# Kernel optimization log

Measured on AMD Instinct MI355X. Metric: run time of the kernel, lower is better.

Reference implementation:

```python
import jax, jax.numpy as jnp
import numpy as np

LEN = 8388608  # 2**23, must be a power of 2


def setup_inputs() -> dict:
    key = jax.random.key(0)
    k1, k2 = jax.random.split(key)
    inp = jax.random.normal(k1, (LEN,), dtype=jnp.float32)
    weight = jax.random.uniform(k2, (LEN // 2, 2), dtype=jnp.float32)  # learned twiddle factors
    return {"input": inp, "weight": weight}


def _complex_mul(a, w):
    # a: [d, cols, 2] complex pairs; w: [cols, 2] broadcast over leading dim
    ar, ai = a[:, :, 0], a[:, :, 1]
    wr, wi = w[:, 0], w[:, 1]
    return jnp.stack([ar * wr - ai * wi, ar * wi + ai * wr], axis=-1)


def reference(input, weight):
    n = input.shape[0]
    # real signal -> complex pairs, shape [n, 1, 2]
    x = jnp.stack([input, jnp.zeros_like(input)], axis=-1)[:, None, :]
    d = n // 2
    while d != 0:  # log2(n) static stages
        w = weight[0::d]          # [cols, 2] where cols == x.shape[1]
        top = x[:d]               # [d, cols, 2]
        bot = x[d:]               # [d, cols, 2]
        p = _complex_mul(bot, w)  # butterfly twiddle multiply
        x = jnp.concatenate([top + p, top - p], axis=1)  # [d, 2*cols, 2]
        d //= 2
    return x  # [1, n, 2]
```

## Files before the change

kernel.cpp:

```cpp
#include <hip/hip_runtime.h>
#include <hip/hip_fp16.h>

typedef float    f4 __attribute__((ext_vector_type(4)));
typedef unsigned u4 __attribute__((ext_vector_type(4)));

__device__ __forceinline__ float2 cadd(float2 a, float2 b) { return make_float2(a.x + b.x, a.y + b.y); }
__device__ __forceinline__ float2 csub(float2 a, float2 b) { return make_float2(a.x - b.x, a.y - b.y); }
__device__ __forceinline__ float2 cmul(float2 w, float2 z) {
    return make_float2(w.x * z.x - w.y * z.y, w.x * z.y + w.y * z.x);
}
__device__ __forceinline__ unsigned pk(float2 z) {
    __half2 h = __floats2half2_rn(z.x, z.y);
    return *reinterpret_cast<unsigned*>(&h);
}
__device__ __forceinline__ float2 upk(unsigned u) {
    __half2 h = *reinterpret_cast<__half2*>(&u);
    return __half22float2(h);
}

__host__ __device__ constexpr unsigned crev(unsigned x, int bits) {
    unsigned r = 0;
    for (int k = 0; k < bits; ++k) r |= ((x >> k) & 1u) << (bits - 1 - k);
    return r;
}


__global__ __launch_bounds__(256) void fft_pass_a(const float* __restrict__ in,
                                                  const float2* __restrict__ wt,
                                                  uint4* __restrict__ outp)
{
    __shared__ float2 L[4096];
    const int tid = threadIdx.x;
    const int l0  = blockIdx.x << 4;
    const int c   = tid & 15;
    const int qb  = tid >> 4;

    float2 pw1[4], pw2a[4], pw2b[4];
#pragma unroll
    for (int k = 0; k < 4; ++k) { pw1[k] = wt[0]; pw2a[k] = wt[0]; pw2b[k] = wt[1 << 21]; }

    {
        const int c4 = tid & 3, gg = tid >> 2;
#pragma unroll
        for (int k = 0; k < 4; ++k) {
            const int g = gg + (k << 6);
            const f4 v = __builtin_nontemporal_load(
                reinterpret_cast<const f4*>(in + ((size_t)g << 15) + l0 + (c4 << 2)));
            const int base = (g << 4) + (c4 << 2);
            L[base + 0] = make_float2(v[0], 0.f);
            L[base + 1] = make_float2(v[1], 0.f);
            L[base + 2] = make_float2(v[2], 0.f);
            L[base + 3] = make_float2(v[3], 0.f);
        }
    }
    __syncthreads();

#pragma unroll
    for (int rho = 0; rho < 4; ++rho) {
        const int s = rho << 1, H = 128 >> s, Q = H >> 1, lo = 6 - s;
        float2 nw1[4], nw2a[4], nw2b[4];
        if (rho < 3) {
            const int s2 = s + 2, lo2 = 6 - s2;
#pragma unroll
            for (int k = 0; k < 4; ++k) {
                const int qi = (qb << 2) + k;
                const int b  = ((qi >> lo2) << (lo2 + 2)) | (qi & ((1 << lo2) - 1));
                const int jl = (int)(__brev((unsigned)(b >> (8 - s2))) >> (32 - s2));
                const int e  = jl << (21 - s2);
                nw1[k] = wt[e << 1]; nw2a[k] = wt[e]; nw2b[k] = wt[e + (1 << 21)];
            }
        }
#pragma unroll
        for (int k = 0; k < 4; ++k) {
            const int qi = (qb << 2) + k;
            const int b  = ((qi >> lo) << (lo + 2)) | (qi & ((1 << lo) - 1));
            const int iA = (b << 4) + c;
            const float2 A  = L[iA];
            const float2 Bv = L[iA + (Q << 4)];
            const float2 Cv = L[iA + (H << 4)];
            const float2 Dv = L[iA + ((H + Q) << 4)];
            const float2 pC = cmul(pw1[k], Cv), pD = cmul(pw1[k], Dv);
            const float2 tA = cadd(A, pC),  tC = csub(A, pC);
            const float2 tB = cadd(Bv, pD), tD = csub(Bv, pD);
            const float2 p2 = cmul(pw2a[k], tB);
            const float2 p3 = cmul(pw2b[k], tD);
            L[iA]                  = cadd(tA, p2);
            L[iA + (Q << 4)]       = csub(tA, p2);
            L[iA + (H << 4)]       = cadd(tC, p3);
            L[iA + ((H + Q) << 4)] = csub(tC, p3);
        }
        __syncthreads();
        if (rho < 3) {
#pragma unroll
            for (int k = 0; k < 4; ++k) { pw1[k] = nw1[k]; pw2a[k] = nw2a[k]; pw2b[k] = nw2b[k]; }
        }
    }

    {
        const int c4 = tid & 3, gg = tid >> 2;
#pragma unroll
        for (int k = 0; k < 4; ++k) {
            const int g  = gg + (k << 6);
            const int li = (g << 4) + (c4 << 2);
            u4 v;
            v[0] = pk(L[li]); v[1] = pk(L[li + 1]); v[2] = pk(L[li + 2]); v[3] = pk(L[li + 3]);
            __builtin_nontemporal_store(v,
                reinterpret_cast<u4*>(&outp[((size_t)g << 13) + (l0 >> 2) + c4]));
        }
    }
}

__global__ __launch_bounds__(256) void fft_pass_b(const unsigned* __restrict__ in,
                                                  const float2* __restrict__ wt,
                                                  unsigned* __restrict__ out)
{
    const int tid = threadIdx.x;
    const int h   = blockIdx.x >> 2;
    const int low = ((blockIdx.x & 3) << 8) | tid;
    const unsigned hrev = __brev((unsigned)h) >> 24;
    const unsigned base = ((unsigned)h << 15) | (unsigned)low;

    float2 X[32];
#pragma unroll
    for (int m = 0; m < 32; ++m)
        X[m] = upk(__builtin_nontemporal_load(&in[base + ((unsigned)m << 10)]));

#pragma unroll
    for (int s = 0; s < 5; ++s) {
        const int half = 1 << (4 - s);
#pragma unroll
        for (int j = 0; j < 16; ++j) {
            const int mh = j >> (4 - s);
            const int lo = (mh << (5 - s)) | (j & (half - 1));
            const int hi = lo | half;
            const unsigned cr = crev((unsigned)mh, s);
            const float2 w = wt[(((cr << 8) | hrev) << (14 - s))];
            const float2 p = cmul(w, X[hi]);
            X[hi] = csub(X[lo], p);
            X[lo] = cadd(X[lo], p);
        }
    }
#pragma unroll
    for (int m = 0; m < 32; ++m)
        __builtin_nontemporal_store(pk(X[m]), &out[base + ((unsigned)m << 10)]);
}

__global__ __launch_bounds__(1024, 8) void fft_pass_c(const uint4* __restrict__ inp4,
                                                      const float2* __restrict__ wt,
                                                      float2* __restrict__ out)
{
    extern __shared__ float2 L[];
    const int tid = threadIdx.x;
    const int bid = blockIdx.x;
    const int h0  = ((bid & 7) << 7) | (bid >> 3);
    const int lam = tid & 7;
    const int bq  = tid >> 3;
    const int R   = (h0 << 3) | lam;

    {
        const int f    = tid & 63;
        const int lm   = (tid >> 6) & 7;
        const int half = tid >> 9;
        const unsigned H = __brev((unsigned)((h0 << 3) | lm)) >> 19;
        const size_t gb = ((size_t)H << 8);
#pragma unroll
        for (int k = 0; k < 2; ++k) {
            const int slot = (half << 7) | (k << 6) | f;
            const u4 v = __builtin_nontemporal_load(
                reinterpret_cast<const u4*>(&inp4[gb + slot]));
            const int base = lm * 1026 + (slot << 2);
            const float2 e0 = upk(v[0]), e1 = upk(v[1]), e2 = upk(v[2]), e3 = upk(v[3]);
            *reinterpret_cast<float4*>(&L[base])     = make_float4(e0.x, e0.y, e1.x, e1.y);
            *reinterpret_cast<float4*>(&L[base + 2]) = make_float4(e2.x, e2.y, e3.x, e3.y);
        }
    }

    float2 w1[2], w2a[2], w2b[2];
#pragma unroll
    for (int k = 0; k < 2; ++k) {
        const int e = R << 8;
        w1[k] = wt[e << 1]; w2a[k] = wt[e]; w2b[k] = wt[e + (1 << 21)];
    }
    float2 f1[2], f2a[2], f2b[2];
    __syncthreads();

#pragma unroll
    for (int rho = 0; rho < 4; ++rho) {
        const int sh = 8 - (rho << 1);
        const int Q  = 1 << sh;
        const int H2 = Q << 1;
        float2 nw1[2], nw2a[2], nw2b[2];
        if (rho < 3) {
            const int rn = rho + 1, shn = 8 - (rn << 1);
#pragma unroll
            for (int k = 0; k < 2; ++k) {
                const int qi = (k << 7) | bq;
                const unsigned ar = (unsigned)(qi >> shn);
                const unsigned xr = __brev(ar) >> (32 - (rn << 1));
                const int e = (int)(((xr << 13) | (unsigned)R) << shn);
                nw1[k] = wt[e << 1]; nw2a[k] = wt[e]; nw2b[k] = wt[e + (1 << 21)];
            }
        } else {
#pragma unroll
            for (int k = 0; k < 2; ++k) {
                const int qi = (k << 7) | bq;
                const unsigned xr = __brev((unsigned)qi) >> 24;
                const int e = (int)((xr << 13) | (unsigned)R);
                f1[k] = wt[e << 1]; f2a[k] = wt[e]; f2b[k] = wt[e + (1 << 21)];
            }
        }
#pragma unroll
        for (int k = 0; k < 2; ++k) {
            const int qi = (k << 7) | bq;
            const int x  = ((qi >> sh) << (sh + 2)) | (qi & (Q - 1));
            const int iA = lam * 1026 + x;
            const float2 A  = L[iA];
            const float2 Bv = L[iA + Q];
            const float2 Cv = L[iA + H2];
            const float2 Dv = L[iA + H2 + Q];
            const float2 pC = cmul(w1[k], Cv), pD = cmul(w1[k], Dv);
            const float2 tA = cadd(A, pC),  tC = csub(A, pC);
            const float2 tB = cadd(Bv, pD), tD = csub(Bv, pD);
            const float2 p2 = cmul(w2a[k], tB);
            const float2 p3 = cmul(w2b[k], tD);
            L[iA]           = cadd(tA, p2);
            L[iA + Q]       = csub(tA, p2);
            L[iA + H2]      = cadd(tC, p3);
            L[iA + H2 + Q]  = csub(tC, p3);
        }
        __syncthreads();
        if (rho < 3) {
#pragma unroll
            for (int k = 0; k < 2; ++k) { w1[k] = nw1[k]; w2a[k] = nw2a[k]; w2b[k] = nw2b[k]; }
        }
    }

    {
#pragma unroll
        for (int k = 0; k < 2; ++k) {
            const int qi = (k << 7) | bq;
            const int x  = qi << 2;
            const int iA = lam * 1026 + x;
            const float4 g0 = *reinterpret_cast<const float4*>(&L[iA]);
            const float4 g1 = *reinterpret_cast<const float4*>(&L[iA + 2]);
            const float2 A  = make_float2(g0.x, g0.y);
            const float2 Bv = make_float2(g0.z, g0.w);
            const float2 Cv = make_float2(g1.x, g1.y);
            const float2 Dv = make_float2(g1.z, g1.w);
            const float2 pC = cmul(f1[k], Cv), pD = cmul(f1[k], Dv);
            const float2 tA = cadd(A, pC),  tC = csub(A, pC);
            const float2 tB = cadd(Bv, pD), tD = csub(Bv, pD);
            const float2 p2 = cmul(f2a[k], tB);
            const float2 p3 = cmul(f2b[k], tD);
            const float2 rA = cadd(tA, p2), rB = csub(tA, p2);
            const float2 rC = cadd(tC, p3), rD = csub(tC, p3);
            *reinterpret_cast<float4*>(&L[iA])     = make_float4(rA.x, rA.y, rB.x, rB.y);
            *reinterpret_cast<float4*>(&L[iA + 2]) = make_float4(rC.x, rC.y, rD.x, rD.y);
        }
    }
    __syncthreads();

    {
        const int l2   = (tid & 3) << 1;
        const int rest = tid >> 2;
#pragma unroll
        for (int k = 0; k < 4; ++k) {
            const int x = (k << 8) | rest;
            const float2 a0 = L[l2 * 1026 + x];
            const float2 a1 = L[(l2 + 1) * 1026 + x];
            const size_t o = ((size_t)(__brev((unsigned)x) >> 22) << 13)
                           | (unsigned)((h0 << 3) | l2);
            f4 sv; sv[0] = a0.x; sv[1] = a0.y; sv[2] = a1.x; sv[3] = a1.y;
            __builtin_nontemporal_store(sv, reinterpret_cast<f4*>(out + o));
        }
    }
}

extern "C" void kernel_launch(void* const* d_in, const int* in_sizes, int n_in,
                              void* d_out, int out_size, void* d_ws, size_t ws_size,
                              hipStream_t stream)
{
    (void)in_sizes; (void)n_in; (void)out_size; (void)ws_size;
    const float*  in = (const float*)d_in[0];
    const float2* wt = (const float2*)d_in[1];
    float2* outc = (float2*)d_out;
    uint4*  buf1 = (uint4*)d_ws;
    unsigned* buf2 = (unsigned*)((char*)d_ws + (32u << 20));

    static bool attr_done = false;
    if (!attr_done) {
        (void)hipFuncSetAttribute(reinterpret_cast<const void*>(fft_pass_c),
                                  hipFuncAttributeMaxDynamicSharedMemorySize, 8 * 1026 * 8);
        attr_done = true;
    }

    fft_pass_a<<<2048, 256, 0, stream>>>(in, wt, buf1);
    fft_pass_b<<<1024, 256, 0, stream>>>((const unsigned*)buf1, wt, buf2);
    fft_pass_c<<<1024, 1024, 8 * 1026 * 8, stream>>>((const uint4*)buf2, wt, outc);
}
```

Before: 201.7 us.

## Rework final FFT pass to one wavefront per row with register and shuffle butterflies

The last FFT pass now gives each 1024-point row to a single 64-lane wavefront. Each lane holds 16 elements in registers, so the first four stages run inside registers and the last six use cross-lane shuffles, instead of radix-4 passes through shared memory with block-wide barriers. Shared memory is kept only for the final transpose and bit-reversed store, and the block size drops to 512 threads. The trade-off is more per-lane twiddle loads, some of them selected per lane, plus higher register pressure and lower thread count per block.

```diff
diff --git a/kernel.cpp b/kernel.cpp
--- a/kernel.cpp
+++ b/kernel.cpp
@@ -22,6 +22,16 @@
     unsigned r = 0;
     for (int k = 0; k < bits; ++k) r |= ((x >> k) & 1u) << (bits - 1 - k);
     return r;
+}
+
+__device__ __forceinline__ float2 sbfly(float2 x, int m, bool hi, float s, float2 wv) {
+    float2 o;
+    o.x = __shfl_xor(x.x, m);
+    o.y = __shfl_xor(x.y, m);
+    const float2 a = hi ? o : x;
+    const float2 b = hi ? x : o;
+    const float2 p = cmul(wv, b);
+    return make_float2(fmaf(s, p.x, a.x), fmaf(s, p.y, a.y));
 }
 
 
@@ -145,127 +155,142 @@
         __builtin_nontemporal_store(pk(X[m]), &out[base + ((unsigned)m << 10)]);
 }
 
-__global__ __launch_bounds__(1024, 8) void fft_pass_c(const uint4* __restrict__ inp4,
-                                                      const float2* __restrict__ wt,
-                                                      float2* __restrict__ out)
+__global__ __launch_bounds__(512, 4) void fft_pass_c(const unsigned* __restrict__ inp,
+                                                     const float2* __restrict__ wt,
+                                                     float2* __restrict__ out)
 {
     extern __shared__ float2 L[];
-    const int tid = threadIdx.x;
-    const int bid = blockIdx.x;
-    const int h0  = ((bid & 7) << 7) | (bid >> 3);
-    const int lam = tid & 7;
-    const int bq  = tid >> 3;
-    const int R   = (h0 << 3) | lam;
-
-    {
-        const int f    = tid & 63;
-        const int lm   = (tid >> 6) & 7;
-        const int half = tid >> 9;
-        const unsigned H = __brev((unsigned)((h0 << 3) | lm)) >> 19;
-        const size_t gb = ((size_t)H << 8);
-#pragma unroll
-        for (int k = 0; k < 2; ++k) {
-            const int slot = (half << 7) | (k << 6) | f;
-            const u4 v = __builtin_nontemporal_load(
-                reinterpret_cast<const u4*>(&inp4[gb + slot]));
-            const int base = lm * 1026 + (slot << 2);
-            const float2 e0 = upk(v[0]), e1 = upk(v[1]), e2 = upk(v[2]), e3 = upk(v[3]);
-            *reinterpret_cast<float4*>(&L[base])     = make_float4(e0.x, e0.y, e1.x, e1.y);
-            *reinterpret_cast<float4*>(&L[base + 2]) = make_float4(e2.x, e2.y, e3.x, e3.y);
-        }
-    }
-
-    float2 w1[2], w2a[2], w2b[2];
-#pragma unroll
-    for (int k = 0; k < 2; ++k) {
-        const int e = R << 8;
-        w1[k] = wt[e << 1]; w2a[k] = wt[e]; w2b[k] = wt[e + (1 << 21)];
-    }
-    float2 f1[2], f2a[2], f2b[2];
-    __syncthreads();
-
-#pragma unroll
-    for (int rho = 0; rho < 4; ++rho) {
-        const int sh = 8 - (rho << 1);
-        const int Q  = 1 << sh;
-        const int H2 = Q << 1;
-        float2 nw1[2], nw2a[2], nw2b[2];
-        if (rho < 3) {
-            const int rn = rho + 1, shn = 8 - (rn << 1);
-#pragma unroll
-            for (int k = 0; k < 2; ++k) {
-                const int qi = (k << 7) | bq;
-                const unsigned ar = (unsigned)(qi >> shn);
-                const unsigned xr = __brev(ar) >> (32 - (rn << 1));
-                const int e = (int)(((xr << 13) | (unsigned)R) << shn);
-                nw1[k] = wt[e << 1]; nw2a[k] = wt[e]; nw2b[k] = wt[e + (1 << 21)];
-            }
-        } else {
-#pragma unroll
-            for (int k = 0; k < 2; ++k) {
-                const int qi = (k << 7) | bq;
-                const unsigned xr = __brev((unsigned)qi) >> 24;
-                const int e = (int)((xr << 13) | (unsigned)R);
-                f1[k] = wt[e << 1]; f2a[k] = wt[e]; f2b[k] = wt[e + (1 << 21)];
-            }
-        }
-#pragma unroll
-        for (int k = 0; k < 2; ++k) {
-            const int qi = (k << 7) | bq;
-            const int x  = ((qi >> sh) << (sh + 2)) | (qi & (Q - 1));
-            const int iA = lam * 1026 + x;
-            const float2 A  = L[iA];
-            const float2 Bv = L[iA + Q];
-            const float2 Cv = L[iA + H2];
-            const float2 Dv = L[iA + H2 + Q];
-            const float2 pC = cmul(w1[k], Cv), pD = cmul(w1[k], Dv);
-            const float2 tA = cadd(A, pC),  tC = csub(A, pC);
-            const float2 tB = cadd(Bv, pD), tD = csub(Bv, pD);
-            const float2 p2 = cmul(w2a[k], tB);
-            const float2 p3 = cmul(w2b[k], tD);
-            L[iA]           = cadd(tA, p2);
-            L[iA + Q]       = csub(tA, p2);
-            L[iA + H2]      = cadd(tC, p3);
-            L[iA + H2 + Q]  = csub(tC, p3);
-        }
-        __syncthreads();
-        if (rho < 3) {
-#pragma unroll
-            for (int k = 0; k < 2; ++k) { w1[k] = nw1[k]; w2a[k] = nw2a[k]; w2b[k] = nw2b[k]; }
-        }
-    }
-
-    {
-#pragma unroll
-        for (int k = 0; k < 2; ++k) {
-            const int qi = (k << 7) | bq;
-            const int x  = qi << 2;
-            const int iA = lam * 1026 + x;
-            const float4 g0 = *reinterpret_cast<const float4*>(&L[iA]);
-            const float4 g1 = *reinterpret_cast<const float4*>(&L[iA + 2]);
-            const float2 A  = make_float2(g0.x, g0.y);
-            const float2 Bv = make_float2(g0.z, g0.w);
-            const float2 Cv = make_float2(g1.x, g1.y);
-            const float2 Dv = make_float2(g1.z, g1.w);
-            const float2 pC = cmul(f1[k], Cv), pD = cmul(f1[k], Dv);
-            const float2 tA = cadd(A, pC),  tC = csub(A, pC);
-            const float2 tB = cadd(Bv, pD), tD = csub(Bv, pD);
-            const float2 p2 = cmul(f2a[k], tB);
-            const float2 p3 = cmul(f2b[k], tD);
-            const float2 rA = cadd(tA, p2), rB = csub(tA, p2);
-            const float2 rC = cadd(tC, p3), rD = csub(tC, p3);
-            *reinterpret_cast<float4*>(&L[iA])     = make_float4(rA.x, rA.y, rB.x, rB.y);
-            *reinterpret_cast<float4*>(&L[iA + 2]) = make_float4(rC.x, rC.y, rD.x, rD.y);
-        }
-    }
+    const int tid  = threadIdx.x;
+    const int bid  = blockIdx.x;
+    const int h0   = ((bid & 7) << 7) | (bid >> 3);
+    const int lane = tid & 63;
+    const int wv_id = tid >> 6;
+    const int R    = __builtin_amdgcn_readfirstlane((h0 << 3) | wv_id);
+    const unsigned H = __brev((unsigned)R) >> 19;
+
+    float2 X[16];
+    {
+        const unsigned gb = (H << 10) + (unsigned)lane;
+#pragma unroll
+        for (int j = 0; j < 16; ++j)
+            X[j] = upk(__builtin_nontemporal_load(&inp[gb + ((unsigned)j << 6)]));
+    }
+
+    {
+        const float2 w13 = wt[(unsigned)R << 9];
+#pragma unroll
+        for (int j = 0; j < 8; ++j) {
+            const float2 p = cmul(w13, X[j + 8]);
+            X[j + 8] = csub(X[j], p);
+            X[j]     = cadd(X[j], p);
+        }
+    }
+#pragma unroll
+    for (int jt = 0; jt < 2; ++jt) {
+        const float2 wv = wt[(((unsigned)jt << 13) | (unsigned)R) << 8];
+#pragma unroll
+        for (int u = 0; u < 4; ++u) {
+            const int lo = (jt << 3) + u, hi = lo + 4;
+            const float2 p = cmul(wv, X[hi]);
+            X[hi] = csub(X[lo], p);
+            X[lo] = cadd(X[lo], p);
+        }
+    }
+#pragma unroll
+    for (int q = 0; q < 4; ++q) {
+        const float2 wv = wt[((crev((unsigned)q, 2) << 13) | (unsigned)R) << 7];
+#pragma unroll
+        for (int u = 0; u < 2; ++u) {
+            const int lo = (q << 2) + u, hi = lo + 2;
+            const float2 p = cmul(wv, X[hi]);
+            X[hi] = csub(X[lo], p);
+            X[lo] = cadd(X[lo], p);
+        }
+    }
+#pragma unroll
+    for (int q = 0; q < 8; ++q) {
+        const float2 wv = wt[((crev((unsigned)q, 3) << 13) | (unsigned)R) << 6];
+        const int lo = q << 1, hi = lo + 1;
+        const float2 p = cmul(wv, X[hi]);
+        X[hi] = csub(X[lo], p);
+        X[lo] = cadd(X[lo], p);
+    }
+
+    {
+        const bool hi = (lane & 32) != 0; const float s = hi ? -1.f : 1.f;
+#pragma unroll
+        for (int j = 0; j < 16; ++j) {
+            const float2 wv = wt[((crev((unsigned)j, 4) << 13) | (unsigned)R) << 5];
+            X[j] = sbfly(X[j], 32, hi, s, wv);
+        }
+    }
+    {
+        const bool hi = (lane & 16) != 0; const float s = hi ? -1.f : 1.f;
+        const int lb5 = lane >> 5;
+#pragma unroll
+        for (int j = 0; j < 16; ++j) {
+            const int base = (int)(((crev((unsigned)j, 4) << 13) | (unsigned)R) << 4);
+            const float2 w0 = wt[base], w1 = wt[base + (1 << 21)];
+            const float2 wv = lb5 ? w1 : w0;
+            X[j] = sbfly(X[j], 16, hi, s, wv);
+        }
+    }
+    {
+        const bool hi = (lane & 8) != 0; const float s = hi ? -1.f : 1.f;
+        const int l4 = (lane >> 4) & 1, l5 = lane >> 5;
+#pragma unroll
+        for (int j = 0; j < 16; ++j) {
+            const int base = (int)(((crev((unsigned)j, 4) << 13) | (unsigned)R) << 3);
+            const float2 s00 = wt[base],             s01 = wt[base + (1 << 20)];
+            const float2 s10 = wt[base + (1 << 21)], s11 = wt[base + (3 << 20)];
+            const float2 wa = l5 ? s01 : s00;
+            const float2 wb = l5 ? s11 : s10;
+            const float2 wv = l4 ? wb : wa;
+            X[j] = sbfly(X[j], 8, hi, s, wv);
+        }
+    }
+    {
+        const bool hi = (lane & 4) != 0; const float s = hi ? -1.f : 1.f;
+#pragma unroll
+        for (int j = 0; j < 16; ++j) {
+            const unsigned xt = ((unsigned)j << 3) | ((unsigned)lane >> 3);
+            const unsigned xr = __brev(xt) >> 25;
+            const float2 wv = wt[((xr << 13) | (unsigned)R) << 2];
+            X[j] = sbfly(X[j], 4, hi, s, wv);
+        }
+    }
+    {
+        const bool hi = (lane & 2) != 0; const float s = hi ? -1.f : 1.f;
+#pragma unroll
+        for (int j = 0; j < 16; ++j) {
+            const unsigned xt = ((unsigned)j << 4) | ((unsigned)lane >> 2);
+            const unsigned xr = __brev(xt) >> 24;
+            const float2 wv = wt[((xr << 13) | (unsigned)R) << 1];
+            X[j] = sbfly(X[j], 2, hi, s, wv);
+        }
+    }
+    {
+        const bool hi = (lane & 1) != 0; const float s = hi ? -1.f : 1.f;
+#pragma unroll
+        for (int j = 0; j < 16; ++j) {
+            const unsigned xt = ((unsigned)j << 5) | ((unsigned)lane >> 1);
+            const unsigned xr = __brev(xt) >> 23;
+            const float2 wv = wt[(xr << 13) | (unsigned)R];
+            X[j] = sbfly(X[j], 1, hi, s, wv);
+        }
+    }
+
+#pragma unroll
+    for (int j = 0; j < 16; ++j)
+        L[wv_id * 1026 + (j << 6) + lane] = X[j];
     __syncthreads();
 
     {
         const int l2   = (tid & 3) << 1;
         const int rest = tid >> 2;
 #pragma unroll
-        for (int k = 0; k < 4; ++k) {
-            const int x = (k << 8) | rest;
+        for (int k = 0; k < 8; ++k) {
+            const int x = (k << 7) | rest;
             const float2 a0 = L[l2 * 1026 + x];
             const float2 a1 = L[(l2 + 1) * 1026 + x];
             const size_t o = ((size_t)(__brev((unsigned)x) >> 22) << 13)
@@ -296,5 +321,5 @@
 
     fft_pass_a<<<2048, 256, 0, stream>>>(in, wt, buf1);
     fft_pass_b<<<1024, 256, 0, stream>>>((const unsigned*)buf1, wt, buf2);
-    fft_pass_c<<<1024, 1024, 8 * 1026 * 8, stream>>>((const uint4*)buf2, wt, outc);
-}
+    fft_pass_c<<<1024, 512, 8 * 1026 * 8, stream>>>((const unsigned*)buf2, wt, outc);
+}
```

Result: slower. 263.2 us (+30.5%).
